# Kernel tuning notes

Hardware: AMD Instinct MI355X
Metric: run time of the kernel (lower is better)

The kernel has to match this reference:

```python
import jax, jax.numpy as jnp
import numpy as np
import math

DEPTH = 3
RATIO = 0.5
EPS = 1e-5


def _mlp_ln(h, W1, b1, W2, b2, W3, b3, g, beta):
    h = jax.nn.gelu(h @ W1 + b1, approximate=False)
    h = jax.nn.gelu(h @ W2 + b2, approximate=False)
    h = h @ W3 + b3
    mu = jnp.mean(h, axis=-1, keepdims=True)
    var = jnp.mean((h - mu) ** 2, axis=-1, keepdims=True)
    return g * (h - mu) * jax.lax.rsqrt(var + EPS) + beta


def _node_to_node(x, s, r, n, p):
    # two-way gather -> scatter_add -> MLP+LN. Row n of x_pad is a zero dummy
    # node that absorbs edges dropped by pooling (fixed-size, jit-friendly).
    x_pad = jnp.concatenate([x, jnp.zeros((1, x.shape[1]), x.dtype)], axis=0)
    msg = x_pad[jnp.concatenate([s, r])]            # [2E, C]
    recv = jnp.concatenate([r, s])                  # [2E]
    agg = jax.ops.segment_sum(msg, recv, num_segments=n + 1)[:n]
    return _mlp_ln(agg, *p)


def _forward(x, senders, receivers, pool_w, down_p, up_p):
    s, r = senders, receivers
    xs, edges, perms = [x], [(s, r)], []
    n = x.shape[0]
    for i in range(DEPTH):
        k = math.ceil(RATIO * n)  # PyG topk: ceil(ratio * N)
        w = pool_w[i]
        score = jnp.tanh(x @ w / jnp.linalg.norm(w))
        vals, perm = jax.lax.top_k(score, k)
        x = x[perm] * vals[:, None]
        # remap edges; dropped nodes (and old dummy n) map to new dummy k
        nmap = jnp.full((n + 1,), k, dtype=s.dtype).at[perm].set(
            jnp.arange(k, dtype=s.dtype))
        ns_, nr_ = nmap[s], nmap[r]
        invalid = (ns_ == k) | (nr_ == k)
        s = jnp.where(invalid, k, ns_)
        r = jnp.where(invalid, k, nr_)
        x = _node_to_node(x, s, r, k, down_p[i])
        if i < DEPTH - 1:
            xs.append(x)
            edges.append((s, r))
        perms.append(perm)
        n = k
    for i in range(DEPTH):
        j = DEPTH - 1 - i
        res = xs[j]
        s, r = edges[j]
        perm = perms[j]
        up = jnp.zeros_like(res).at[perm].set(x)
        x = jnp.concatenate([res, up], axis=-1)  # sum_res=False -> concat
        x = _node_to_node(x, s, r, res.shape[0], up_p[i])
    return x


def setup_inputs() -> dict:
    key = jax.random.key(0)
    ks = jax.random.split(key, 16)
    N, E, C, D = 50000, 600000, 128, DEPTH
    f32 = jnp.float32

    def lin(k, fi, fo):
        return (jax.random.normal(k, (D, fi, fo), f32) / np.sqrt(fi)).astype(f32)

    return {
        'x': jax.random.normal(ks[0], (N, C), f32),
        'senders': jax.random.randint(ks[1], (E,), 0, N, dtype=jnp.int32),
        'receivers': jax.random.randint(ks[2], (E,), 0, N, dtype=jnp.int32),
        'pool_w': jax.random.normal(ks[3], (D, C), f32),
        'down_W1': lin(ks[4], C, C), 'down_b1': jnp.zeros((D, C), f32),
        'down_W2': lin(ks[5], C, C), 'down_b2': jnp.zeros((D, C), f32),
        'down_W3': lin(ks[6], C, C), 'down_b3': jnp.zeros((D, C), f32),
        'down_g': jnp.ones((D, C), f32), 'down_beta': jnp.zeros((D, C), f32),
        'up_W1': lin(ks[7], 2 * C, C), 'up_b1': jnp.zeros((D, C), f32),
        'up_W2': lin(ks[8], C, C), 'up_b2': jnp.zeros((D, C), f32),
        'up_W3': lin(ks[9], C, C), 'up_b3': jnp.zeros((D, C), f32),
        'up_g': jnp.ones((D, C), f32), 'up_beta': jnp.zeros((D, C), f32),
    }


def reference(x, senders, receivers, pool_w,
              down_W1, down_b1, down_W2, down_b2, down_W3, down_b3,
              down_g, down_beta,
              up_W1, up_b1, up_W2, up_b2, up_W3, up_b3, up_g, up_beta):
    down_p = [(down_W1[i], down_b1[i], down_W2[i], down_b2[i],
               down_W3[i], down_b3[i], down_g[i], down_beta[i])
              for i in range(DEPTH)]
    up_p = [(up_W1[i], up_b1[i], up_W2[i], up_b2[i],
             up_W3[i], up_b3[i], up_g[i], up_beta[i])
            for i in range(DEPTH)]
    return _forward(x, senders, receivers, pool_w, down_p, up_p)
```

## Files before the change

kernel.cpp:

```cpp
#include <hip/hip_runtime.h>
#include <math.h>


typedef unsigned short u16;
typedef short bf16x8 __attribute__((ext_vector_type(8)));
typedef float f32x4 __attribute__((ext_vector_type(4)));

#define HIST_STRIDE (2 * 65536 + 512)
#define NB 128
#define NB_LOG 7
#define SUBR 5000

__device__ __forceinline__ unsigned int fkey(float f) {
  unsigned int b = __float_as_uint(f);
  return (b & 0x80000000u) ? ~b : (b | 0x80000000u);
}

__device__ __forceinline__ float gelu_f(float v) {
  return 0.5f * v * (1.0f + erff(v * 0.70710678118654752f));
}

__device__ __forceinline__ u16 f2bf(float f) {
  unsigned u = __float_as_uint(f);
  u = (u + 0x7FFFu + ((u >> 16) & 1u)) >> 16;
// ... 190 lines not shown
                                  int* __restrict__ nmap, int n, int k) {
  __shared__ int red[256];
  __shared__ int woff[4];
  int t = threadIdx.x;
  red[t] = (t < (int)blockIdx.x) ? tcnt[t] : 0;
  __syncthreads();
  for (int s = 128; s; s >>= 1) {
    if (t < s) red[t] += red[t + s];
    __syncthreads();
  }
  int blockbase = red[0];
  unsigned uT = (unsigned)meta[3];
  int tsel = meta[4];
  int i = blockIdx.x * 256 + t;
  unsigned u = (i < n) ? fkey(key[i]) : 0u;
  bool tie = (i < n) && (u == uT);
  unsigned long long m = __ballot(tie);
  int lane = t & 63, w = t >> 6;
  if (lane == 0) woff[w] = __popcll(m);
  __syncthreads();
  if (t == 0) {
    int c = 0;
    for (int q = 0; q < 4; ++q) { int v = woff[q]; woff[q] = c; c += v; }
  }
  __syncthreads();
  if (i > n) return;
  if (i == n) { nmap[n] = k; return; }
  bool sel;
  if (tie) {
    int pre = __popcll(m & ((1ull << lane) - 1ull));
    int rank = blockbase + woff[w] + pre;
    sel = (rank < tsel);
  } else {
    sel = (u > uT);
  }
  if (sel) {
    int slot = atomicAdd(&meta[5], 1);
    perm[slot] = i; vals[slot] = valt[i]; nmap[i] = slot;
  } else {
    nmap[i] = k;
  }
}

__global__ void pool_kernel(const float* __restrict__ x, const int* __restrict__ perm,
                            const float* __restrict__ vals, float* __restrict__ xp, int k) {
  int gid = blockIdx.x * 256 + threadIdx.x;
  int t = gid >> 5;
  if (t >= k) return;
  int c = (gid & 31) << 2;
  float v = vals[t];
  float4 a = *(const float4*)&x[(size_t)perm[t] * 128 + c];
  a.x *= v; a.y *= v; a.z *= v; a.w *= v;
  *(float4*)&xp[(size_t)t * 128 + c] = a;
}

__global__ void csr_count_kernel(const int* __restrict__ s, const int* __restrict__ r,
                                 int* __restrict__ H, int N, int E, int CH) {
  __shared__ int cnt[SUBR];
  int b = blockIdx.x & (NB - 1);
  int sub = blockIdx.x >> NB_LOG;
  int base = sub * SUBR;
  int top = base + SUBR; if (top > N) top = N;
  int span = top - base;
  for (int t = threadIdx.x; t < span; t += 256) cnt[t] = 0;
  __syncthreads();
  int lo = b * CH, hi = lo + CH; if (hi > E) hi = E;
  for (int e = lo + threadIdx.x; e < hi; e += 256) {
    int sv = s[e], rv = r[e];
    if ((unsigned)(rv - base) < (unsigned)span) atomicAdd(&cnt[rv - base], 1);
    if ((unsigned)(sv - base) < (unsigned)span) atomicAdd(&cnt[sv - base], 1);
  }
  __syncthreads();
  int* Hb = H + (size_t)b * N + base;
  for (int t = threadIdx.x; t < span; t += 256) Hb[t] = cnt[t];
}

__global__ void colsum_part_kernel(const int* __restrict__ H, int* __restrict__ deg,
                                   int* __restrict__ bsum, int n) {
  __shared__ int l[256];
  int i = blockIdx.x * 256 + threadIdx.x;
  int v = 0;
  if (i < n) {
#pragma unroll 4
    for (int b = 0; b < NB; ++b) v += H[(size_t)b * n + i];
    deg[i] = v;
  }
  l[threadIdx.x] = (i < n) ? v : 0;
  __syncthreads();
  for (int s = 128; s; s >>= 1) {
    if (threadIdx.x < s) l[threadIdx.x] += l[threadIdx.x + s];
    __syncthreads();
  }
  if (threadIdx.x == 0) bsum[blockIdx.x] = l[0];
}

__global__ void scanfix_kernel(const int* __restrict__ deg, const int* __restrict__ bsum,
                               int* __restrict__ off, int* __restrict__ H, int n) {
  __shared__ int red[256];
  __shared__ int l[256];
  int i = blockIdx.x * 256 + threadIdx.x;
  int t = threadIdx.x;
  red[t] = (t < (int)blockIdx.x) ? bsum[t] : 0;
  __syncthreads();
  for (int s = 128; s; s >>= 1) {
    if (t < s) red[t] += red[t + s];
    __syncthreads();
  }
  int base = red[0];
  int v = (i < n) ? deg[i] : 0;
  l[t] = v;
  __syncthreads();
#pragma unroll
  for (int s = 1; s < 256; s <<= 1) {
    int add = (t >= s) ? l[t - s] : 0;
    __syncthreads();
    l[t] += add;
    __syncthreads();
  }
  int incl = l[t];
  if (i < n) {
    int e = base + incl - v;
    off[i] = e;
    if (i == n - 1) off[n] = base + incl;
    int run = e;
#pragma unroll 4
    for (int b = 0; b < NB; ++b) {
      size_t id = (size_t)b * n + i;
      int tv = H[id];
      H[id] = run;
      run += tv;
    }
  }
}

__global__ void csr_scatter_lds_kernel(const int* __restrict__ s, const int* __restrict__ r,
                                       const int* __restrict__ H, int* __restrict__ idx,
                                       int N, int E, int CH) {
  __shared__ int cnt[SUBR];
  int b = blockIdx.x & (NB - 1);
  int sub = blockIdx.x >> NB_LOG;
  int base = sub * SUBR;
  int top = base + SUBR; if (top > N) top = N;
  int span = top - base;
  for (int t = threadIdx.x; t < span; t += 256) cnt[t] = 0;
  __syncthreads();
  int lo = b * CH, hi = lo + CH; if (hi > E) hi = E;
  const int* Hb = H + (size_t)b * N;
  for (int e = lo + threadIdx.x; e < hi; e += 256) {
    int sv = s[e], rv = r[e];
    if ((unsigned)(rv - base) < (unsigned)span) {
      int loc = atomicAdd(&cnt[rv - base], 1);
      idx[Hb[rv] + loc] = sv;
    }
    if ((unsigned)(sv - base) < (unsigned)span) {
      int loc = atomicAdd(&cnt[sv - base], 1);
      idx[Hb[sv] + loc] = rv;
    }
  }
}

__global__ void derive_deg_kernel(const int* __restrict__ permL, const int* __restrict__ nm,
                                  const int* __restrict__ offP, const int* __restrict__ idxP,
                                  int* __restrict__ deg, int k) {
  int wave = threadIdx.x >> 6, lane = threadIdx.x & 63;
  int v = blockIdx.x * 4 + wave;
  if (v >= k) return;
  int p = permL[v];
  int lo = __builtin_amdgcn_readfirstlane(offP[p]);
  int hi = __builtin_amdgcn_readfirstlane(offP[p + 1]);
  int cnt = 0;
  for (int j0 = lo; j0 < hi; j0 += 64) {
    int j = j0 + lane;
    bool ok = (j < hi) && (nm[idxP[j]] < k);
    unsigned long long msk = __ballot(ok);
    cnt += __popcll(msk);
  }
  if (lane == 0) deg[v] = cnt;
}

__global__ void derive_fill_kernel(const int* __restrict__ permL, const int* __restrict__ nm,
                                   const int* __restrict__ offP, const int* __restrict__ idxP,
                                   const int* __restrict__ offL, int* __restrict__ idxL,
                                   int k) {
  int wave = threadIdx.x >> 6, lane = threadIdx.x & 63;
  int v = blockIdx.x * 4 + wave;
  if (v >= k) return;
  int p = permL[v];
  int lo = __builtin_amdgcn_readfirstlane(offP[p]);
  int hi = __builtin_amdgcn_readfirstlane(offP[p + 1]);
  int base = __builtin_amdgcn_readfirstlane(offL[v]);
  for (int j0 = lo; j0 < hi; j0 += 64) {
    int j = j0 + lane;
    int m = k;
    if (j < hi) m = nm[idxP[j]];
    bool ok = m < k;
    unsigned long long msk = __ballot(ok);
    int rank = __popcll(msk & ((1ull << lane) - 1ull));
    if (ok) idxL[base + rank] = m;
    base += __popcll(msk);
  }
}

__global__ void scan_part_kernel(const int* __restrict__ deg, int* __restrict__ bsum, int n) {
  __shared__ int l[256];
  int i = blockIdx.x * 256 + threadIdx.x;
  l[threadIdx.x] = (i < n) ? deg[i] : 0;
  __syncthreads();
  for (int s = 128; s; s >>= 1) {
    if (threadIdx.x < s) l[threadIdx.x] += l[threadIdx.x + s];
    __syncthreads();
  }
  if (threadIdx.x == 0) bsum[blockIdx.x] = l[0];
}

__global__ void scan_final_kernel(const int* __restrict__ deg, const int* __restrict__ bsum,
                                  int* __restrict__ off, int n) {
  __shared__ int red[256];
  __shared__ int l[256];
  int i = blockIdx.x * 256 + threadIdx.x;
  int t = threadIdx.x;
  red[t] = (t < (int)blockIdx.x) ? bsum[t] : 0;
  __syncthreads();
  for (int s = 128; s; s >>= 1) {
    if (t < s) red[t] += red[t + s];
    __syncthreads();
  }
  int base = red[0];
  int v = (i < n) ? deg[i] : 0;
  l[t] = v;
  __syncthreads();
#pragma unroll
  for (int s = 1; s < 256; s <<= 1) {
    int add = (t >= s) ? l[t - s] : 0;
    __syncthreads();
    l[t] += add;
    __syncthreads();
  }
  int incl = l[t];
  if (i < n) {
    int e = base + incl - v;
    off[i] = e;
    if (i == n - 1) off[n] = base + incl;
  }
}

__global__ void idxup3_kernel(const int* __restrict__ idxA, const int* __restrict__ nmA,
                              const int* __restrict__ lenA, int* __restrict__ outA,
                              const int* __restrict__ idxB, const int* __restrict__ nmB,
                              const int* __restrict__ lenB, int* __restrict__ outB,
                              const int* __restrict__ idxC, const int* __restrict__ nmC,
                              const int* __restrict__ lenC, int* __restrict__ outC,
                              int nbSeg, int maxlen) {
  int seg = blockIdx.x / nbSeg;
  int j = (blockIdx.x - seg * nbSeg) * 256 + threadIdx.x;
  if (j >= maxlen) return;
  const int* idx; const int* nm; const int* len; int* out;
  if (seg == 0)      { idx = idxA; nm = nmA; len = lenA; out = outA; }
  else if (seg == 1) { idx = idxB; nm = nmB; len = lenB; out = outB; }
  else               { idx = idxC; nm = nmC; len = lenC; out = outC; }
  if (j >= len[0]) return;
  out[j] = nm[idx[j]];
}

__global__ void agg_kernel(const float* __restrict__ x, const int* __restrict__ off,
                           const int* __restrict__ idx, float* __restrict__ agg, int n) {
  int wave = threadIdx.x >> 6, lane = threadIdx.x & 63;
  int v = blockIdx.x * 4 + wave;
  if (v >= n) return;
  int lo = __builtin_amdgcn_readfirstlane(off[v]);
  int hi = __builtin_amdgcn_readfirstlane(off[v + 1]);
  int g = lane >> 5, sl = lane & 31;
  const float* bp = x + sl * 4;
  float4 acc = {0.f, 0.f, 0.f, 0.f};
#define ACC_F(EE)                                        \
  do {                                                   \
    float4 w_ = *(const float4*)(bp + (size_t)(EE) * 128);\
    acc.x += w_.x; acc.y += w_.y; acc.z += w_.z; acc.w += w_.w; \
  } while (0)
  int j = lo;
  for (; j + 8 <= hi; j += 8) {
    int q0 = idx[j],     q1 = idx[j + 1], q2 = idx[j + 2], q3 = idx[j + 3];
    int q4 = idx[j + 4], q5 = idx[j + 5], q6 = idx[j + 6], q7 = idx[j + 7];
    ACC_F(g ? q1 : q0);
    ACC_F(g ? q3 : q2);
    ACC_F(g ? q5 : q4);
    ACC_F(g ? q7 : q6);
  }
  for (; j + 2 <= hi; j += 2) {
    int q0 = idx[j], q1 = idx[j + 1];
    ACC_F(g ? q1 : q0);
  }
  if (j < hi) {
    int q0 = idx[j];
    if (!g) ACC_F(q0);
  }
#undef ACC_F
  acc.x += __shfl_xor(acc.x, 32, 64);
  acc.y += __shfl_xor(acc.y, 32, 64);
  acc.z += __shfl_xor(acc.z, 32, 64);
  acc.w += __shfl_xor(acc.w, 32, 64);
  if (!g) *(float4*)&agg[(size_t)v * 128 + sl * 4] = acc;
}

template <int OFS>
__global__ void agg_gather_kernel(const u16* __restrict__ tab, const int* __restrict__ idx,
                                  const int* __restrict__ off, u16* __restrict__ agg, int n) {
  int wave = threadIdx.x >> 6, lane = threadIdx.x & 63;
  int v = blockIdx.x * 4 + wave;
  if (v >= n) return;
  int lo = __builtin_amdgcn_readfirstlane(off[v]);
  int hi = __builtin_amdgcn_readfirstlane(off[v + 1]);
  int g = lane >> 4, sl = lane & 15;
  const u16* bp = tab + sl * 8;
  float4 a0 = {0.f, 0.f, 0.f, 0.f}, a1 = {0.f, 0.f, 0.f, 0.f};

#define ACC_ROW(EE)                                     \
  do {                                                  \
    uint4 wq = *(const uint4*)(bp + (size_t)(EE) * 128);\
    a0.x += __uint_as_float(wq.x << 16);                \
    a0.y += __uint_as_float(wq.x & 0xffff0000u);        \
    a0.z += __uint_as_float(wq.y << 16);                \
    a0.w += __uint_as_float(wq.y & 0xffff0000u);        \
    a1.x += __uint_as_float(wq.z << 16);                \
    a1.y += __uint_as_float(wq.z & 0xffff0000u);        \
    a1.z += __uint_as_float(wq.w << 16);                \
    a1.w += __uint_as_float(wq.w & 0xffff0000u);        \
  } while (0)

  int j = lo;
  for (; j + 16 <= hi; j += 16) {
    int e0 = idx[j + g];
    int e1 = idx[j + g + 4];
    int e2 = idx[j + g + 8];
    int e3 = idx[j + g + 12];
    ACC_ROW(e0); ACC_ROW(e1); ACC_ROW(e2); ACC_ROW(e3);
  }
  for (; j + 4 <= hi; j += 4) {
    int e0 = idx[j + g];
    ACC_ROW(e0);
  }
  int rmn = hi - j;
  if (g < rmn) {
    int e = idx[j + g];
    ACC_ROW(e);
  }
#undef ACC_ROW

  a0.x += __shfl_xor(a0.x, 16, 64);
  a0.y += __shfl_xor(a0.y, 16, 64);
  a0.z += __shfl_xor(a0.z, 16, 64);
  a0.w += __shfl_xor(a0.w, 16, 64);
  a1.x += __shfl_xor(a1.x, 16, 64);
  a1.y += __shfl_xor(a1.y, 16, 64);
  a1.z += __shfl_xor(a1.z, 16, 64);
  a1.w += __shfl_xor(a1.w, 16, 64);
  a0.x += __shfl_xor(a0.x, 32, 64);
  a0.y += __shfl_xor(a0.y, 32, 64);
  a0.z += __shfl_xor(a0.z, 32, 64);
  a0.w += __shfl_xor(a0.w, 32, 64);
  a1.x += __shfl_xor(a1.x, 32, 64);
  a1.y += __shfl_xor(a1.y, 32, 64);
  a1.z += __shfl_xor(a1.z, 32, 64);
  a1.w += __shfl_xor(a1.w, 32, 64);

  if (lane < 16) {
    bf16x8 ov;
    ov[0] = (short)f2bf(a0.x); ov[1] = (short)f2bf(a0.y);
    ov[2] = (short)f2bf(a0.z); ov[3] = (short)f2bf(a0.w);
    ov[4] = (short)f2bf(a1.x); ov[5] = (short)f2bf(a1.y);
    ov[6] = (short)f2bf(a1.z); ov[7] = (short)f2bf(a1.w);
    *(bf16x8*)&agg[(size_t)v * 256 + OFS + sl * 8] = ov;
  }
}

template <bool GELU>
__global__ __launch_bounds__(256) void gemm_kernel(const float* __restrict__ A,
                                                   const float* __restrict__ W,
                                                   const float* __restrict__ bias,
                                                   float* __restrict__ out, int n) {
  __shared__ float As[32 * 32];
  __shared__ float Ws[32 * 128];
  int t = threadIdx.x;
  int row0 = blockIdx.x * 32;
  int colg = (t & 31) << 2;
  int rowg = (t >> 5) << 2;
  float acc[4][4];
#pragma unroll
  for (int i = 0; i < 4; ++i)
#pragma unroll
    for (int j = 0; j < 4; ++j) acc[i][j] = 0.f;

  for (int k0 = 0; k0 < 128; k0 += 32) {
    __syncthreads();
    {
      int ar = t >> 3, ac = (t & 7) << 2;
      float4 av = make_float4(0.f, 0.f, 0.f, 0.f);
      if (row0 + ar < n) av = *(const float4*)&A[(size_t)(row0 + ar) * 128 + k0 + ac];
      *(float4*)&As[ar * 32 + ac] = av;
    }
#pragma unroll
    for (int l = 0; l < 4; ++l) {
      int id = t + l * 256;
      int kk = id >> 5, wc = (id & 31) << 2;
      *(float4*)&Ws[kk * 128 + wc] = *(const float4*)&W[(size_t)(k0 + kk) * 128 + wc];
    }
    __syncthreads();
#pragma unroll
    for (int kk = 0; kk < 32; kk += 4) {
      float4 wv[4];
#pragma unroll
      for (int j = 0; j < 4; ++j) wv[j] = *(const float4*)&Ws[(kk + j) * 128 + colg];
#pragma unroll
      for (int i = 0; i < 4; ++i) {
        float4 av = *(const float4*)&As[(rowg + i) * 32 + kk];
        acc[i][0] += av.x * wv[0].x + av.y * wv[1].x + av.z * wv[2].x + av.w * wv[3].x;
        acc[i][1] += av.x * wv[0].y + av.y * wv[1].y + av.z * wv[2].y + av.w * wv[3].y;
        acc[i][2] += av.x * wv[0].z + av.y * wv[1].z + av.z * wv[2].z + av.w * wv[3].z;
        acc[i][3] += av.x * wv[0].w + av.y * wv[1].w + av.z * wv[2].w + av.w * wv[3].w;
      }
    }
  }
  float4 bv = *(const float4*)&bias[colg];
#pragma unroll
  for (int i = 0; i < 4; ++i) {
    int rr = row0 + rowg + i;
    if (rr < n) {
      float4 o = make_float4(acc[i][0] + bv.x, acc[i][1] + bv.y, acc[i][2] + bv.z, acc[i][3] + bv.w);
      if (GELU) { o.x = gelu_f(o.x); o.y = gelu_f(o.y); o.z = gelu_f(o.z); o.w = gelu_f(o.w); }
      *(float4*)&out[(size_t)rr * 128 + colg] = o;
    }
  }
}

template <int K>
__global__ __launch_bounds__(256) void gemm_mfma_kernel(const u16* __restrict__ A,
                                                        const u16* __restrict__ WT,
                                                        const float* __restrict__ bias,
                                                        u16* __restrict__ out, int n) {
  __shared__ u16 As[64 * 72];
  __shared__ u16 Ws[128 * 72];
  int t = threadIdx.x;
  int lane = t & 63, wave = t >> 6;
  int row0 = blockIdx.x * 64;
  f32x4 acc[8];
#pragma unroll
  for (int i = 0; i < 8; ++i) acc[i] = (f32x4){0.f, 0.f, 0.f, 0.f};

  for (int k0 = 0; k0 < K; k0 += 64) {
    __syncthreads();
#pragma unroll
    for (int i = 0; i < 2; ++i) {
      int c = t + i * 256;
      int r = c >> 3, seg = c & 7;
      bf16x8 v = {0, 0, 0, 0, 0, 0, 0, 0};
      if (row0 + r < n) v = *(const bf16x8*)&A[(size_t)(row0 + r) * K + k0 + seg * 8];
      *(bf16x8*)&As[r * 72 + seg * 8] = v;
    }
#pragma unroll
    for (int i = 0; i < 4; ++i) {
      int c = t + i * 256;
      int r = c >> 3, seg = c & 7;
      *(bf16x8*)&Ws[r * 72 + seg * 8] = *(const bf16x8*)&WT[(size_t)r * K + k0 + seg * 8];
    }
    __syncthreads();
#pragma unroll
    for (int kk = 0; kk < 64; kk += 32) {
      bf16x8 a = *(const bf16x8*)&As[(wave * 16 + (lane & 15)) * 72 + kk + (lane >> 4) * 8];
#pragma unroll
      for (int ct = 0; ct < 8; ++ct) {
        bf16x8 b = *(const bf16x8*)&Ws[(ct * 16 + (lane & 15)) * 72 + kk + (lane >> 4) * 8];
        acc[ct] = __builtin_amdgcn_mfma_f32_16x16x32_bf16(a, b, acc[ct], 0, 0, 0);
      }
    }
  }
  int colb = lane & 15, rquad = lane >> 4;
#pragma unroll
  for (int ct = 0; ct < 8; ++ct) {
#pragma unroll
    for (int r = 0; r < 4; ++r) {
      int row = row0 + wave * 16 + rquad * 4 + r;
      if (row < n) {
        int col = ct * 16 + colb;
        out[(size_t)row * 128 + col] = f2bf(gelu_f(acc[ct][r] + bias[col]));
      }
    }
  }
}

template <bool WF32, bool WBF>
__global__ __launch_bounds__(256) void gemm_mfma_ln_kernel(
    const u16* __restrict__ A, const u16* __restrict__ WT, const float* __restrict__ bias,
    const float* __restrict__ g, const float* __restrict__ beta,
    float* __restrict__ out, u16* __restrict__ outbf, int n) {
  __shared__ u16 As[64 * 72];
  __shared__ u16 Ws[128 * 72];
  int t = threadIdx.x;
  int lane = t & 63, wave = t >> 6;
  int row0 = blockIdx.x * 64;
  f32x4 acc[8];
#pragma unroll
  for (int i = 0; i < 8; ++i) acc[i] = (f32x4){0.f, 0.f, 0.f, 0.f};

  for (int k0 = 0; k0 < 128; k0 += 64) {
    __syncthreads();
#pragma unroll
    for (int i = 0; i < 2; ++i) {
      int c = t + i * 256;
      int r = c >> 3, seg = c & 7;
      bf16x8 v = {0, 0, 0, 0, 0, 0, 0, 0};
      if (row0 + r < n) v = *(const bf16x8*)&A[(size_t)(row0 + r) * 128 + k0 + seg * 8];
      *(bf16x8*)&As[r * 72 + seg * 8] = v;
    }
#pragma unroll
    for (int i = 0; i < 4; ++i) {
      int c = t + i * 256;
      int r = c >> 3, seg = c & 7;
      *(bf16x8*)&Ws[r * 72 + seg * 8] = *(const bf16x8*)&WT[(size_t)r * 128 + k0 + seg * 8];
    }
    __syncthreads();
#pragma unroll
    for (int kk = 0; kk < 64; kk += 32) {
      bf16x8 a = *(const bf16x8*)&As[(wave * 16 + (lane & 15)) * 72 + kk + (lane >> 4) * 8];
#pragma unroll
      for (int ct = 0; ct < 8; ++ct) {
        bf16x8 b = *(const bf16x8*)&Ws[(ct * 16 + (lane & 15)) * 72 + kk + (lane >> 4) * 8];
        acc[ct] = __builtin_amdgcn_mfma_f32_16x16x32_bf16(a, b, acc[ct], 0, 0, 0);
      }
    }
  }
  int colb = lane & 15, rquad = lane >> 4;
  float bv[8], gv[8], bev[8];
#pragma unroll
  for (int ct = 0; ct < 8; ++ct) {
    int col = ct * 16 + colb;
    bv[ct] = bias[col]; gv[ct] = g[col]; bev[ct] = beta[col];
  }
#pragma unroll
  for (int r = 0; r < 4; ++r) {
    float s1 = 0.f;
#pragma unroll
    for (int ct = 0; ct < 8; ++ct) s1 += acc[ct][r] + bv[ct];
#pragma unroll
    for (int o = 1; o <= 8; o <<= 1) s1 += __shfl_xor(s1, o, 64);
    float mu = s1 * (1.0f / 128.0f);
    float s2 = 0.f;
#pragma unroll
    for (int ct = 0; ct < 8; ++ct) { float d = acc[ct][r] + bv[ct] - mu; s2 += d * d; }
#pragma unroll
    for (int o = 1; o <= 8; o <<= 1) s2 += __shfl_xor(s2, o, 64);
    float rs = rsqrtf(s2 * (1.0f / 128.0f) + 1e-5f);
    int row = row0 + wave * 16 + rquad * 4 + r;
    if (row < n) {
#pragma unroll
      for (int ct = 0; ct < 8; ++ct) {
        int col = ct * 16 + colb;
        float o = gv[ct] * (acc[ct][r] + bv[ct] - mu) * rs + bev[ct];
        if (WF32) out[(size_t)row * 128 + col] = o;
        if (WBF)  outbf[(size_t)row * 128 + col] = f2bf(o);
      }
    }
  }
}

template <bool SCORE, bool WBF>
__global__ void ln_kernel(const float* __restrict__ h, const float* __restrict__ g,
                          const float* __restrict__ beta, float* __restrict__ out,
                          u16* __restrict__ outbf, const float* __restrict__ wnext,
                          const double* __restrict__ sqn, float* __restrict__ key,
                          float* __restrict__ valt, int n) {
  int wave = threadIdx.x >> 6, lane = threadIdx.x & 63;
  int i = blockIdx.x * 4 + wave;
  if (i >= n) return;
  float2 hv = *(const float2*)&h[(size_t)i * 128 + lane * 2];
  float s = hv.x + hv.y;
  for (int o = 32; o; o >>= 1) s += __shfl_down(s, o, 64);
  float mu = __shfl(s, 0, 64) * (1.0f / 128.0f);
  float dx = hv.x - mu, dy = hv.y - mu;
  float q = dx * dx + dy * dy;
  for (int o = 32; o; o >>= 1) q += __shfl_down(q, o, 64);
  float var = __shfl(q, 0, 64) * (1.0f / 128.0f);
  float rs = rsqrtf(var + 1e-5f);
  float2 gv = *(const float2*)&g[lane * 2];
  float2 bv = *(const float2*)&beta[lane * 2];
  float2 o2; o2.x = gv.x * dx * rs + bv.x; o2.y = gv.y * dy * rs + bv.y;
  *(float2*)&out[(size_t)i * 128 + lane * 2] = o2;
  if (WBF)
    *(ushort2*)&outbf[(size_t)i * 128 + lane * 2] = make_ushort2(f2bf(o2.x), f2bf(o2.y));
  if (SCORE) {
    float2 wv = *(const float2*)&wnext[lane * 2];
    double d = (double)o2.x * wv.x + (double)o2.y * wv.y;
    for (int o = 32; o; o >>= 1) d += __shfl_down(d, o, 64);
    if (lane == 0) {
      key[i]  = (float)d;
      valt[i] = (float)tanh(d / sqn[0]);
    }
  }
}


static inline int cdiv(int a, int b) { return (a + b - 1) / b; }

extern "C" void kernel_launch(void* const* d_in, const int* in_sizes, int n_in,
                              void* d_out, int out_size, void* d_ws, size_t ws_size,
                              hipStream_t stream) {
  const float* x0   = (const float*)d_in[0];
  const int*   snd  = (const int*)d_in[1];
  const int*   rcv  = (const int*)d_in[2];
  const float* poolw = (const float*)d_in[3];
  const float* dW1 = (const float*)d_in[4];
  const float* db1 = (const float*)d_in[5];
  const float* dW2 = (const float*)d_in[6];
  const float* db2 = (const float*)d_in[7];
  const float* dW3 = (const float*)d_in[8];
  const float* db3 = (const float*)d_in[9];
  const float* dg  = (const float*)d_in[10];
  const float* dbe = (const float*)d_in[11];
  const float* uW1 = (const float*)d_in[12];
  const float* ub1 = (const float*)d_in[13];
  const float* uW2 = (const float*)d_in[14];
  const float* ub2 = (const float*)d_in[15];
  const float* uW3 = (const float*)d_in[16];
  const float* ub3 = (const float*)d_in[17];
  const float* ug  = (const float*)d_in[18];
  const float* ube = (const float*)d_in[19];

  const int N0 = in_sizes[0] / 128;
  const int E  = in_sizes[1];
  const int N1 = (N0 + 1) / 2, N2 = (N1 + 1) / 2, N3 = (N2 + 1) / 2;

  char* p = (char*)d_ws;
  auto alloc = [&](size_t bytes) -> void* {
    void* r = (void*)p;
    p += (bytes + 255) & ~(size_t)255;
    return r;
  };
  float* key  = (float*)alloc((size_t)N0 * 4);
  float* valt = (float*)alloc((size_t)N0 * 4);
  int*   histAll = (int*)alloc((size_t)3 * HIST_STRIDE * 4);
  int*   meta = (int*)alloc(64 * 4);
  int*   tcnt = (int*)alloc(512 * 4);
  int*   bsum = (int*)alloc(256 * 4);
  int*   nm1 = (int*)alloc((size_t)(N0 + 1) * 4);
  int*   nm2 = (int*)alloc((size_t)(N1 + 1) * 4);
  int*   nm3 = (int*)alloc((size_t)(N2 + 1) * 4);
  int*   perm0 = (int*)alloc((size_t)N1 * 4);
  int*   perm1 = (int*)alloc((size_t)N2 * 4);
  int*   perm2 = (int*)alloc((size_t)N3 * 4);
  float* vals  = (float*)alloc((size_t)N1 * 4);
  double* sqn  = (double*)alloc(8 * 8);
  float* x1 = (float*)alloc((size_t)N1 * 128 * 4);
  float* x2 = (float*)alloc((size_t)N2 * 128 * 4);
  float* x3 = (float*)alloc((size_t)N3 * 128 * 4);
  float* xp = (float*)alloc((size_t)N1 * 128 * 4);
  float* aggf = (float*)alloc((size_t)N1 * 128 * 4);
  float* h1f  = (float*)alloc((size_t)N1 * 128 * 4);
  float* h2f  = (float*)alloc((size_t)N1 * 128 * 4);
  u16* agg_bf = (u16*)alloc((size_t)N0 * 256 * 2);
  u16* res0_bf = (u16*)alloc((size_t)N0 * 128 * 2);
  u16* res1_bf = (u16*)alloc((size_t)N1 * 128 * 2);
  u16* res2_bf = (u16*)alloc((size_t)N2 * 128 * 2);
  u16* x3_bf   = (u16*)alloc((size_t)(N3 + 1) * 128 * 2);
  u16* xu2_bf  = (u16*)alloc((size_t)(N2 + 1) * 128 * 2);
  u16* xu1_bf  = (u16*)alloc((size_t)(N1 + 1) * 128 * 2);
  u16* wt1 = (u16*)alloc((size_t)3 * 128 * 256 * 2);
  u16* wt2 = (u16*)alloc((size_t)3 * 128 * 128 * 2);
  u16* wt3 = (u16*)alloc((size_t)3 * 128 * 128 * 2);
  int* degAll = (int*)alloc((size_t)(N0 + N1 + N2 + N3) * 4);
  int* deg0 = degAll;
  int* deg1 = degAll + N0;
  int* deg2 = deg1 + N1;
  int* deg3 = deg2 + N2;
  int* off0 = (int*)alloc((size_t)(N0 + 1) * 4);
  int* idx0 = (int*)alloc((size_t)2 * E * 4);
  int* off1 = (int*)alloc((size_t)(N1 + 1) * 4);
  int* idx1 = (int*)alloc((size_t)2 * E * 4);
  int* off2 = (int*)alloc((size_t)(N2 + 1) * 4);
  int* idx2 = (int*)alloc((size_t)2 * E * 4);
  int* off3 = (int*)alloc((size_t)(N3 + 1) * 4);
  int* idx3 = (int*)alloc((size_t)2 * E * 4);
  int* idxu0 = (int*)alloc((size_t)2 * E * 4);
  int* idxu1 = (int*)alloc((size_t)2 * E * 4);
  int* idxu2 = (int*)alloc((size_t)2 * E * 4);
  int* H = (int*)alloc((size_t)NB * N0 * 4);
  u16* h1b = (u16*)xp;
  u16* h2b = (u16*)alloc((size_t)N0 * 128 * 2);

  auto run_scan = [&](int* degB, int* offB, int n) {
    int nb = cdiv(n, 256);
    scan_part_kernel<<<nb, 256, 0, stream>>>(degB, bsum, n);
    scan_final_kernel<<<nb, 256, 0, stream>>>(degB, bsum, offB, n);
  };

  {
    int nbX = cdiv(N0 * 32, 256);
    int nHist = 3 * HIST_STRIDE;
    int nbHZ = cdiv(nHist, 256);
    preamble_kernel<<<nbX + 768 + 1 + 1 + nbHZ, 256, 0, stream>>>(
        x0, res0_bf, N0, uW1, uW2, uW3, wt1, wt2, wt3, poolw, sqn,
        x3_bf + (size_t)N3 * 128, xu2_bf + (size_t)N2 * 128,
        xu1_bf + (size_t)N1 * 128, histAll, nbX, nbHZ, nHist);
  }

  {
    int nSub = cdiv(N0, SUBR);
    int CH = cdiv(E, NB);
    int nbN = cdiv(N0, 256);
    csr_count_kernel<<<NB * nSub, 256, 0, stream>>>(snd, rcv, H, N0, E, CH);
    colsum_part_kernel<<<nbN, 256, 0, stream>>>(H, deg0, bsum, N0);
    scanfix_kernel<<<nbN, 256, 0, stream>>>(deg0, bsum, off0, H, N0);
    csr_scatter_lds_kernel<<<NB * nSub, 256, 0, stream>>>(snd, rcv, H, idx0, N0, E, CH);
  }

  auto down_step = [&](int n, int k, const float* xcur, int* permL, int* nmL,
                       float* xnext, u16* xnext_bf, int lvl,
                       const int* offP, const int* idxP,
                       int* offL, int* degL, int* idxL) {
    int nb = cdiv(n, 256);
    int* histL = histAll + (size_t)lvl * HIST_STRIDE;
    int* csum_hi = histL + 2 * 65536;
    int* csum_lo = csum_hi + 256;
    hist_hi_kernel<<<nb, 256, 0, stream>>>(key, histL, csum_hi, n);
    find_hi2_kernel<<<1, 256, 0, stream>>>(histL, csum_hi, meta, k);
    hist_lo_kernel<<<nb, 256, 0, stream>>>(key, meta, histL + 65536, csum_lo, n);
    find_lo2_kernel<<<1, 256, 0, stream>>>(histL + 65536, csum_lo, meta);
    tie_count_kernel<<<nb, 256, 0, stream>>>(key, meta, tcnt, n);
    tie_select_kernel<<<cdiv(n + 1, 256), 256, 0, stream>>>(
        key, valt, tcnt, meta, permL, vals, nmL, n, k);
    pool_kernel<<<cdiv(k * 32, 256), 256, 0, stream>>>(xcur, permL, vals, xp, k);
    derive_deg_kernel<<<cdiv(k, 4), 256, 0, stream>>>(permL, nmL, offP, idxP, degL, k);
    run_scan(degL, offL, k);
    derive_fill_kernel<<<cdiv(k, 4), 256, 0, stream>>>(permL, nmL, offP, idxP, offL, idxL, k);
    agg_kernel<<<cdiv(k, 4), 256, 0, stream>>>(xp, offL, idxL, aggf, k);
    gemm_kernel<true><<<cdiv(k, 32), 256, 0, stream>>>(
        aggf, dW1 + (size_t)lvl * 128 * 128, db1 + (size_t)lvl * 128, h1f, k);
    gemm_kernel<true><<<cdiv(k, 32), 256, 0, stream>>>(
        h1f, dW2 + (size_t)lvl * 128 * 128, db2 + (size_t)lvl * 128, h2f, k);
    gemm_kernel<false><<<cdiv(k, 32), 256, 0, stream>>>(
        h2f, dW3 + (size_t)lvl * 128 * 128, db3 + (size_t)lvl * 128, h1f, k);
    if (lvl < 2)
      ln_kernel<true, true><<<cdiv(k, 4), 256, 0, stream>>>(
          h1f, dg + (size_t)lvl * 128, dbe + (size_t)lvl * 128, xnext, xnext_bf,
          poolw + (size_t)(lvl + 1) * 128, sqn + (lvl + 1), key, valt, k);
    else
      ln_kernel<false, true><<<cdiv(k, 4), 256, 0, stream>>>(
          h1f, dg + (size_t)lvl * 128, dbe + (size_t)lvl * 128, xnext, xnext_bf,
          nullptr, nullptr, nullptr, nullptr, k);
  };

  score_kernel<<<cdiv(N0, 4), 256, 0, stream>>>(x0, poolw, key, valt, N0);
  down_step(N0, N1, x0, perm0, nm1, x1, res1_bf, 0, off0, idx0, off1, deg1, idx1);
  down_step(N1, N2, x1, perm1, nm2, x2, res2_bf, 1, off1, idx1, off2, deg2, idx2);
  down_step(N2, N3, x2, perm2, nm3, x3, x3_bf,   2, off2, idx2, off3, deg3, idx3);

  {
    int nbSeg = cdiv(2 * E, 256);
    idxup3_kernel<<<3 * nbSeg, 256, 0, stream>>>(
        idx2, nm3, off2 + N2, idxu2,
        idx1, nm2, off1 + N1, idxu1,
        idx0, nm1, off0 + N0, idxu0, nbSeg, 2 * E);
  }

  auto up_step = [&](int n, const u16* resb, const u16* xdb, int lvl,
                     const int* offL, const int* idxL, const int* idxUL,
                     bool wantF32, float* outF32, u16* outBF) {
    agg_gather_kernel<0><<<cdiv(n, 4), 256, 0, stream>>>(resb, idxL, offL, agg_bf, n);
    agg_gather_kernel<128><<<cdiv(n, 4), 256, 0, stream>>>(xdb, idxUL, offL, agg_bf, n);
    gemm_mfma_kernel<256><<<cdiv(n, 64), 256, 0, stream>>>(
        agg_bf, wt1 + (size_t)lvl * 128 * 256, ub1 + (size_t)lvl * 128, h1b, n);
    gemm_mfma_kernel<128><<<cdiv(n, 64), 256, 0, stream>>>(
        h1b, wt2 + (size_t)lvl * 128 * 128, ub2 + (size_t)lvl * 128, h2b, n);
    if (wantF32)
      gemm_mfma_ln_kernel<true, false><<<cdiv(n, 64), 256, 0, stream>>>(
          h2b, wt3 + (size_t)lvl * 128 * 128, ub3 + (size_t)lvl * 128,
          ug + (size_t)lvl * 128, ube + (size_t)lvl * 128, outF32, nullptr, n);
    else
      gemm_mfma_ln_kernel<false, true><<<cdiv(n, 64), 256, 0, stream>>>(
          h2b, wt3 + (size_t)lvl * 128 * 128, ub3 + (size_t)lvl * 128,
          ug + (size_t)lvl * 128, ube + (size_t)lvl * 128, nullptr, outBF, n);
  };

  up_step(N2, res2_bf, x3_bf,  0, off2, idx2, idxu2, false, nullptr, xu2_bf);
  up_step(N1, res1_bf, xu2_bf, 1, off1, idx1, idxu1, false, nullptr, xu1_bf);
  up_step(N0, res0_bf, xu1_bf, 2, off0, idx0, idxu0, true, (float*)d_out, nullptr);

  (void)n_in; (void)out_size; (void)ws_size;
}
```

Measured before the change: 831.2 us.

## Fuse three-layer MLP and LayerNorm into single kernels for down and up paths

The down path now runs one kernel that chains all three fp32 GEMMs, GELU, LayerNorm and the next-level score computation, keeping intermediates in shared memory. The up path does the same with bf16 MFMA, holding hidden activations in LDS instead of round-tripping through global buffers. The two gather launches per up level are also merged into one grid. This removes several launches and global reads and writes of intermediates. In exchange it uses more LDS per block, which may lower occupancy, and reduces the LayerNorm across 32 lanes with shuffles.

```diff
diff --git a/kernel.cpp b/kernel.cpp
--- a/kernel.cpp
+++ b/kernel.cpp
@@ -516,11 +516,17 @@
   if (!g) *(float4*)&agg[(size_t)v * 128 + sl * 4] = acc;
 }
 
-template <int OFS>
-__global__ void agg_gather_kernel(const u16* __restrict__ tab, const int* __restrict__ idx,
-                                  const int* __restrict__ off, u16* __restrict__ agg, int n) {
+__global__ void agg_gather2_kernel(const u16* __restrict__ tabR, const int* __restrict__ idxR,
+                                   const u16* __restrict__ tabU, const int* __restrict__ idxU,
+                                   const int* __restrict__ off, u16* __restrict__ agg,
+                                   int n, int nbHalf) {
+  bool upH = (int)blockIdx.x >= nbHalf;
+  int blk = upH ? (int)blockIdx.x - nbHalf : (int)blockIdx.x;
+  const u16* tab = upH ? tabU : tabR;
+  const int* idx = upH ? idxU : idxR;
+  int OFS = upH ? 128 : 0;
   int wave = threadIdx.x >> 6, lane = threadIdx.x & 63;
-  int v = blockIdx.x * 4 + wave;
+  int v = blk * 4 + wave;
   if (v >= n) return;
   int lo = __builtin_amdgcn_readfirstlane(off[v]);
   int hi = __builtin_amdgcn_readfirstlane(off[v + 1]);
@@ -587,11 +593,17 @@
   }
 }
 
-template <bool GELU>
-__global__ __launch_bounds__(256) void gemm_kernel(const float* __restrict__ A,
-                                                   const float* __restrict__ W,
-                                                   const float* __restrict__ bias,
-                                                   float* __restrict__ out, int n) {
+template <bool SCORE>
+__global__ __launch_bounds__(256) void mlp_down_kernel(
+    const float* __restrict__ A,
+    const float* __restrict__ W1, const float* __restrict__ b1,
+    const float* __restrict__ W2, const float* __restrict__ b2,
+    const float* __restrict__ W3, const float* __restrict__ b3,
+    const float* __restrict__ g, const float* __restrict__ beta,
+    float* __restrict__ out, u16* __restrict__ outbf,
+    const float* __restrict__ wnext, const double* __restrict__ sqn,
+    float* __restrict__ key, float* __restrict__ valt, int n) {
+  __shared__ float cur[32 * 128];
   __shared__ float As[32 * 32];
   __shared__ float Ws[32 * 128];
   int t = threadIdx.x;
@@ -599,82 +611,138 @@
   int colg = (t & 31) << 2;
   int rowg = (t >> 5) << 2;
   float acc[4][4];
-#pragma unroll
-  for (int i = 0; i < 4; ++i)
-#pragma unroll
-    for (int j = 0; j < 4; ++j) acc[i][j] = 0.f;
-
-  for (int k0 = 0; k0 < 128; k0 += 32) {
-    __syncthreads();
-    {
-      int ar = t >> 3, ac = (t & 7) << 2;
-      float4 av = make_float4(0.f, 0.f, 0.f, 0.f);
-      if (row0 + ar < n) av = *(const float4*)&A[(size_t)(row0 + ar) * 128 + k0 + ac];
-      *(float4*)&As[ar * 32 + ac] = av;
-    }
-#pragma unroll
-    for (int l = 0; l < 4; ++l) {
-      int id = t + l * 256;
-      int kk = id >> 5, wc = (id & 31) << 2;
-      *(float4*)&Ws[kk * 128 + wc] = *(const float4*)&W[(size_t)(k0 + kk) * 128 + wc];
-    }
-    __syncthreads();
-#pragma unroll
-    for (int kk = 0; kk < 32; kk += 4) {
-      float4 wv[4];
-#pragma unroll
-      for (int j = 0; j < 4; ++j) wv[j] = *(const float4*)&Ws[(kk + j) * 128 + colg];
+  const float* Wl[3] = {W1, W2, W3};
+  const float* bl[3] = {b1, b2, b3};
+#pragma unroll
+  for (int l = 0; l < 3; ++l) {
+    const float* W = Wl[l];
+#pragma unroll
+    for (int i = 0; i < 4; ++i)
+#pragma unroll
+      for (int j = 0; j < 4; ++j) acc[i][j] = 0.f;
+    for (int k0 = 0; k0 < 128; k0 += 32) {
+      __syncthreads();
+      {
+        int ar = t >> 3, ac = (t & 7) << 2;
+        float4 av;
+        if (l == 0) {
+          av = make_float4(0.f, 0.f, 0.f, 0.f);
+          if (row0 + ar < n) av = *(const float4*)&A[(size_t)(row0 + ar) * 128 + k0 + ac];
+        } else {
+          av = *(const float4*)&cur[ar * 128 + k0 + ac];
+        }
+        *(float4*)&As[ar * 32 + ac] = av;
+      }
+#pragma unroll
+      for (int ll = 0; ll < 4; ++ll) {
+        int id = t + ll * 256;
+        int kk = id >> 5, wc = (id & 31) << 2;
+        *(float4*)&Ws[kk * 128 + wc] = *(const float4*)&W[(size_t)(k0 + kk) * 128 + wc];
+      }
+      __syncthreads();
+#pragma unroll
+      for (int kk = 0; kk < 32; kk += 4) {
+        float4 wv[4];
+#pragma unroll
+        for (int j = 0; j < 4; ++j) wv[j] = *(const float4*)&Ws[(kk + j) * 128 + colg];
+#pragma unroll
+        for (int i = 0; i < 4; ++i) {
+          float4 av = *(const float4*)&As[(rowg + i) * 32 + kk];
+          acc[i][0] += av.x * wv[0].x + av.y * wv[1].x + av.z * wv[2].x + av.w * wv[3].x;
+          acc[i][1] += av.x * wv[0].y + av.y * wv[1].y + av.z * wv[2].y + av.w * wv[3].y;
+          acc[i][2] += av.x * wv[0].z + av.y * wv[1].z + av.z * wv[2].z + av.w * wv[3].z;
+          acc[i][3] += av.x * wv[0].w + av.y * wv[1].w + av.z * wv[2].w + av.w * wv[3].w;
+        }
+      }
+    }
+    float4 bv = *(const float4*)&bl[l][colg];
+    if (l < 2) {
+      __syncthreads();
 #pragma unroll
       for (int i = 0; i < 4; ++i) {
-        float4 av = *(const float4*)&As[(rowg + i) * 32 + kk];
-        acc[i][0] += av.x * wv[0].x + av.y * wv[1].x + av.z * wv[2].x + av.w * wv[3].x;
-        acc[i][1] += av.x * wv[0].y + av.y * wv[1].y + av.z * wv[2].y + av.w * wv[3].y;
-        acc[i][2] += av.x * wv[0].z + av.y * wv[1].z + av.z * wv[2].z + av.w * wv[3].z;
-        acc[i][3] += av.x * wv[0].w + av.y * wv[1].w + av.z * wv[2].w + av.w * wv[3].w;
+        float4 o = make_float4(gelu_f(acc[i][0] + bv.x), gelu_f(acc[i][1] + bv.y),
+                               gelu_f(acc[i][2] + bv.z), gelu_f(acc[i][3] + bv.w));
+        *(float4*)&cur[(rowg + i) * 128 + colg] = o;
       }
-    }
-  }
-  float4 bv = *(const float4*)&bias[colg];
+    } else {
+#pragma unroll
+      for (int i = 0; i < 4; ++i) {
+        acc[i][0] += bv.x; acc[i][1] += bv.y; acc[i][2] += bv.z; acc[i][3] += bv.w;
+      }
+    }
+  }
+  float4 gvv = *(const float4*)&g[colg];
+  float4 bev = *(const float4*)&beta[colg];
+  float4 wv4 = make_float4(0.f, 0.f, 0.f, 0.f);
+  if (SCORE) wv4 = *(const float4*)&wnext[colg];
 #pragma unroll
   for (int i = 0; i < 4; ++i) {
+    float s1 = acc[i][0] + acc[i][1] + acc[i][2] + acc[i][3];
+#pragma unroll
+    for (int o = 1; o <= 16; o <<= 1) s1 += __shfl_xor(s1, o, 64);
+    float mu = s1 * (1.0f / 128.0f);
+    float d0 = acc[i][0] - mu, d1 = acc[i][1] - mu, d2 = acc[i][2] - mu, d3 = acc[i][3] - mu;
+    float s2 = d0 * d0 + d1 * d1 + d2 * d2 + d3 * d3;
+#pragma unroll
+    for (int o = 1; o <= 16; o <<= 1) s2 += __shfl_xor(s2, o, 64);
+    float rs = rsqrtf(s2 * (1.0f / 128.0f) + 1e-5f);
     int rr = row0 + rowg + i;
+    float o0 = gvv.x * d0 * rs + bev.x;
+    float o1 = gvv.y * d1 * rs + bev.y;
+    float o2 = gvv.z * d2 * rs + bev.z;
+    float o3 = gvv.w * d3 * rs + bev.w;
     if (rr < n) {
-      float4 o = make_float4(acc[i][0] + bv.x, acc[i][1] + bv.y, acc[i][2] + bv.z, acc[i][3] + bv.w);
-      if (GELU) { o.x = gelu_f(o.x); o.y = gelu_f(o.y); o.z = gelu_f(o.z); o.w = gelu_f(o.w); }
-      *(float4*)&out[(size_t)rr * 128 + colg] = o;
-    }
-  }
-}
-
-template <int K>
-__global__ __launch_bounds__(256) void gemm_mfma_kernel(const u16* __restrict__ A,
-                                                        const u16* __restrict__ WT,
-                                                        const float* __restrict__ bias,
-                                                        u16* __restrict__ out, int n) {
+      *(float4*)&out[(size_t)rr * 128 + colg] = make_float4(o0, o1, o2, o3);
+      *(ushort4*)&outbf[(size_t)rr * 128 + colg] =
+          make_ushort4(f2bf(o0), f2bf(o1), f2bf(o2), f2bf(o3));
+    }
+    if (SCORE) {
+      double d = (double)o0 * wv4.x + (double)o1 * wv4.y +
+                 (double)o2 * wv4.z + (double)o3 * wv4.w;
+#pragma unroll
+      for (int o = 1; o <= 16; o <<= 1) d += __shfl_xor(d, o, 64);
+      if ((t & 31) == 0 && rr < n) {
+        key[rr]  = (float)d;
+        valt[rr] = (float)tanh(d / sqn[0]);
+      }
+    }
+  }
+}
+
+template <bool WF32, bool WBF>
+__global__ __launch_bounds__(256) void mlp_up_kernel(
+    const u16* __restrict__ A,
+    const u16* __restrict__ WT1, const float* __restrict__ b1,
+    const u16* __restrict__ WT2, const float* __restrict__ b2,
+    const u16* __restrict__ WT3, const float* __restrict__ b3,
+    const float* __restrict__ g, const float* __restrict__ beta,
+    float* __restrict__ out, u16* __restrict__ outbf, int n) {
   __shared__ u16 As[64 * 72];
   __shared__ u16 Ws[128 * 72];
+  __shared__ u16 cur[64 * 136];
   int t = threadIdx.x;
   int lane = t & 63, wave = t >> 6;
   int row0 = blockIdx.x * 64;
+  int colb = lane & 15, rquad = lane >> 4;
   f32x4 acc[8];
+
 #pragma unroll
   for (int i = 0; i < 8; ++i) acc[i] = (f32x4){0.f, 0.f, 0.f, 0.f};
-
-  for (int k0 = 0; k0 < K; k0 += 64) {
+  for (int k0 = 0; k0 < 256; k0 += 64) {
     __syncthreads();
 #pragma unroll
     for (int i = 0; i < 2; ++i) {
       int c = t + i * 256;
       int r = c >> 3, seg = c & 7;
       bf16x8 v = {0, 0, 0, 0, 0, 0, 0, 0};
-      if (row0 + r < n) v = *(const bf16x8*)&A[(size_t)(row0 + r) * K + k0 + seg * 8];
+      if (row0 + r < n) v = *(const bf16x8*)&A[(size_t)(row0 + r) * 256 + k0 + seg * 8];
       *(bf16x8*)&As[r * 72 + seg * 8] = v;
     }
 #pragma unroll
     for (int i = 0; i < 4; ++i) {
       int c = t + i * 256;
       int r = c >> 3, seg = c & 7;
-      *(bf16x8*)&Ws[r * 72 + seg * 8] = *(const bf16x8*)&WT[(size_t)r * K + k0 + seg * 8];
+      *(bf16x8*)&Ws[r * 72 + seg * 8] = *(const bf16x8*)&WT1[(size_t)r * 256 + k0 + seg * 8];
     }
     __syncthreads();
 #pragma unroll
@@ -687,54 +755,32 @@
       }
     }
   }
-  int colb = lane & 15, rquad = lane >> 4;
+  __syncthreads();
 #pragma unroll
   for (int ct = 0; ct < 8; ++ct) {
+    int col = ct * 16 + colb;
+    float bb = b1[col];
 #pragma unroll
     for (int r = 0; r < 4; ++r) {
-      int row = row0 + wave * 16 + rquad * 4 + r;
-      if (row < n) {
-        int col = ct * 16 + colb;
-        out[(size_t)row * 128 + col] = f2bf(gelu_f(acc[ct][r] + bias[col]));
-      }
-    }
-  }
-}
-
-template <bool WF32, bool WBF>
-__global__ __launch_bounds__(256) void gemm_mfma_ln_kernel(
-    const u16* __restrict__ A, const u16* __restrict__ WT, const float* __restrict__ bias,
-    const float* __restrict__ g, const float* __restrict__ beta,
-    float* __restrict__ out, u16* __restrict__ outbf, int n) {
-  __shared__ u16 As[64 * 72];
-  __shared__ u16 Ws[128 * 72];
-  int t = threadIdx.x;
-  int lane = t & 63, wave = t >> 6;
-  int row0 = blockIdx.x * 64;
-  f32x4 acc[8];
+      int row = wave * 16 + rquad * 4 + r;
+      cur[row * 136 + col] = f2bf(gelu_f(acc[ct][r] + bb));
+    }
+  }
+
 #pragma unroll
   for (int i = 0; i < 8; ++i) acc[i] = (f32x4){0.f, 0.f, 0.f, 0.f};
-
   for (int k0 = 0; k0 < 128; k0 += 64) {
     __syncthreads();
-#pragma unroll
-    for (int i = 0; i < 2; ++i) {
-      int c = t + i * 256;
-      int r = c >> 3, seg = c & 7;
-      bf16x8 v = {0, 0, 0, 0, 0, 0, 0, 0};
-      if (row0 + r < n) v = *(const bf16x8*)&A[(size_t)(row0 + r) * 128 + k0 + seg * 8];
-      *(bf16x8*)&As[r * 72 + seg * 8] = v;
-    }
 #pragma unroll
     for (int i = 0; i < 4; ++i) {
       int c = t + i * 256;
       int r = c >> 3, seg = c & 7;
-      *(bf16x8*)&Ws[r * 72 + seg * 8] = *(const bf16x8*)&WT[(size_t)r * 128 + k0 + seg * 8];
+      *(bf16x8*)&Ws[r * 72 + seg * 8] = *(const bf16x8*)&WT2[(size_t)r * 128 + k0 + seg * 8];
     }
     __syncthreads();
 #pragma unroll
     for (int kk = 0; kk < 64; kk += 32) {
-      bf16x8 a = *(const bf16x8*)&As[(wave * 16 + (lane & 15)) * 72 + kk + (lane >> 4) * 8];
+      bf16x8 a = *(const bf16x8*)&cur[(wave * 16 + (lane & 15)) * 136 + k0 + kk + (lane >> 4) * 8];
 #pragma unroll
       for (int ct = 0; ct < 8; ++ct) {
         bf16x8 b = *(const bf16x8*)&Ws[(ct * 16 + (lane & 15)) * 72 + kk + (lane >> 4) * 8];
@@ -742,12 +788,44 @@
       }
     }
   }
-  int colb = lane & 15, rquad = lane >> 4;
-  float bv[8], gv[8], bev[8];
+  __syncthreads();
 #pragma unroll
   for (int ct = 0; ct < 8; ++ct) {
     int col = ct * 16 + colb;
-    bv[ct] = bias[col]; gv[ct] = g[col]; bev[ct] = beta[col];
+    float bb = b2[col];
+#pragma unroll
+    for (int r = 0; r < 4; ++r) {
+      int row = wave * 16 + rquad * 4 + r;
+      cur[row * 136 + col] = f2bf(gelu_f(acc[ct][r] + bb));
+    }
+  }
+
+#pragma unroll
+  for (int i = 0; i < 8; ++i) acc[i] = (f32x4){0.f, 0.f, 0.f, 0.f};
+  for (int k0 = 0; k0 < 128; k0 += 64) {
+    __syncthreads();
+#pragma unroll
+    for (int i = 0; i < 4; ++i) {
+      int c = t + i * 256;
+      int r = c >> 3, seg = c & 7;
+      *(bf16x8*)&Ws[r * 72 + seg * 8] = *(const bf16x8*)&WT3[(size_t)r * 128 + k0 + seg * 8];
+    }
+    __syncthreads();
+#pragma unroll
+    for (int kk = 0; kk < 64; kk += 32) {
+      bf16x8 a = *(const bf16x8*)&cur[(wave * 16 + (lane & 15)) * 136 + k0 + kk + (lane >> 4) * 8];
+#pragma unroll
+      for (int ct = 0; ct < 8; ++ct) {
+        bf16x8 b = *(const bf16x8*)&Ws[(ct * 16 + (lane & 15)) * 72 + kk + (lane >> 4) * 8];
+        acc[ct] = __builtin_amdgcn_mfma_f32_16x16x32_bf16(a, b, acc[ct], 0, 0, 0);
+      }
+    }
+  }
+  float bv[8], gv[8], bev[8];
+#pragma unroll
+  for (int ct = 0; ct < 8; ++ct) {
+    int col = ct * 16 + colb;
+    bv[ct] = b3[col]; gv[ct] = g[col]; bev[ct] = beta[col];
   }
 #pragma unroll
   for (int r = 0; r < 4; ++r) {
@@ -772,41 +850,6 @@
         if (WF32) out[(size_t)row * 128 + col] = o;
         if (WBF)  outbf[(size_t)row * 128 + col] = f2bf(o);
       }
-    }
-  }
-}
-
-template <bool SCORE, bool WBF>
-__global__ void ln_kernel(const float* __restrict__ h, const float* __restrict__ g,
-                          const float* __restrict__ beta, float* __restrict__ out,
-                          u16* __restrict__ outbf, const float* __restrict__ wnext,
-                          const double* __restrict__ sqn, float* __restrict__ key,
-                          float* __restrict__ valt, int n) {
-  int wave = threadIdx.x >> 6, lane = threadIdx.x & 63;
-  int i = blockIdx.x * 4 + wave;
-  if (i >= n) return;
-  float2 hv = *(const float2*)&h[(size_t)i * 128 + lane * 2];
-  float s = hv.x + hv.y;
-  for (int o = 32; o; o >>= 1) s += __shfl_down(s, o, 64);
-  float mu = __shfl(s, 0, 64) * (1.0f / 128.0f);
-  float dx = hv.x - mu, dy = hv.y - mu;
-  float q = dx * dx + dy * dy;
-  for (int o = 32; o; o >>= 1) q += __shfl_down(q, o, 64);
-  float var = __shfl(q, 0, 64) * (1.0f / 128.0f);
-  float rs = rsqrtf(var + 1e-5f);
-  float2 gv = *(const float2*)&g[lane * 2];
-  float2 bv = *(const float2*)&beta[lane * 2];
-  float2 o2; o2.x = gv.x * dx * rs + bv.x; o2.y = gv.y * dy * rs + bv.y;
-  *(float2*)&out[(size_t)i * 128 + lane * 2] = o2;
-  if (WBF)
-    *(ushort2*)&outbf[(size_t)i * 128 + lane * 2] = make_ushort2(f2bf(o2.x), f2bf(o2.y));
-  if (SCORE) {
-    float2 wv = *(const float2*)&wnext[lane * 2];
-    double d = (double)o2.x * wv.x + (double)o2.y * wv.y;
-    for (int o = 32; o; o >>= 1) d += __shfl_down(d, o, 64);
-    if (lane == 0) {
-      key[i]  = (float)d;
-      valt[i] = (float)tanh(d / sqn[0]);
     }
   }
 }
@@ -867,8 +910,6 @@
   float* x3 = (float*)alloc((size_t)N3 * 128 * 4);
   float* xp = (float*)alloc((size_t)N1 * 128 * 4);
   float* aggf = (float*)alloc((size_t)N1 * 128 * 4);
-  float* h1f  = (float*)alloc((size_t)N1 * 128 * 4);
-  float* h2f  = (float*)alloc((size_t)N1 * 128 * 4);
   u16* agg_bf = (u16*)alloc((size_t)N0 * 256 * 2);
   u16* res0_bf = (u16*)alloc((size_t)N0 * 128 * 2);
   u16* res1_bf = (u16*)alloc((size_t)N1 * 128 * 2);
@@ -896,14 +937,6 @@
   int* idxu1 = (int*)alloc((size_t)2 * E * 4);
   int* idxu2 = (int*)alloc((size_t)2 * E * 4);
   int* H = (int*)alloc((size_t)NB * N0 * 4);
-  u16* h1b = (u16*)xp;
-  u16* h2b = (u16*)alloc((size_t)N0 * 128 * 2);
-
-  auto run_scan = [&](int* degB, int* offB, int n) {
-    int nb = cdiv(n, 256);
-    scan_part_kernel<<<nb, 256, 0, stream>>>(degB, bsum, n);
-    scan_final_kernel<<<nb, 256, 0, stream>>>(degB, bsum, offB, n);
-  };
 
   {
     int nbX = cdiv(N0 * 32, 256);
@@ -924,6 +957,12 @@
     scanfix_kernel<<<nbN, 256, 0, stream>>>(deg0, bsum, off0, H, N0);
     csr_scatter_lds_kernel<<<NB * nSub, 256, 0, stream>>>(snd, rcv, H, idx0, N0, E, CH);
   }
+
+  auto run_scan = [&](int* degB, int* offB, int n) {
+    int nb = cdiv(n, 256);
+    scan_part_kernel<<<nb, 256, 0, stream>>>(degB, bsum, n);
+    scan_final_kernel<<<nb, 256, 0, stream>>>(degB, bsum, offB, n);
+  };
 
   auto down_step = [&](int n, int k, const float* xcur, int* permL, int* nmL,
                        float* xnext, u16* xnext_bf, int lvl,
@@ -945,20 +984,23 @@
     run_scan(degL, offL, k);
     derive_fill_kernel<<<cdiv(k, 4), 256, 0, stream>>>(permL, nmL, offP, idxP, offL, idxL, k);
     agg_kernel<<<cdiv(k, 4), 256, 0, stream>>>(xp, offL, idxL, aggf, k);
-    gemm_kernel<true><<<cdiv(k, 32), 256, 0, stream>>>(
-        aggf, dW1 + (size_t)lvl * 128 * 128, db1 + (size_t)lvl * 128, h1f, k);
-    gemm_kernel<true><<<cdiv(k, 32), 256, 0, stream>>>(
-        h1f, dW2 + (size_t)lvl * 128 * 128, db2 + (size_t)lvl * 128, h2f, k);
-    gemm_kernel<false><<<cdiv(k, 32), 256, 0, stream>>>(
-        h2f, dW3 + (size_t)lvl * 128 * 128, db3 + (size_t)lvl * 128, h1f, k);
     if (lvl < 2)
-      ln_kernel<true, true><<<cdiv(k, 4), 256, 0, stream>>>(
-          h1f, dg + (size_t)lvl * 128, dbe + (size_t)lvl * 128, xnext, xnext_bf,
-          poolw + (size_t)(lvl + 1) * 128, sqn + (lvl + 1), key, valt, k);
+      mlp_down_kernel<true><<<cdiv(k, 32), 256, 0, stream>>>(
+          aggf,
+          dW1 + (size_t)lvl * 128 * 128, db1 + (size_t)lvl * 128,
+          dW2 + (size_t)lvl * 128 * 128, db2 + (size_t)lvl * 128,
+          dW3 + (size_t)lvl * 128 * 128, db3 + (size_t)lvl * 128,
+          dg + (size_t)lvl * 128, dbe + (size_t)lvl * 128,
+          xnext, xnext_bf, poolw + (size_t)(lvl + 1) * 128, sqn + (lvl + 1),
+          key, valt, k);
     else
-      ln_kernel<false, true><<<cdiv(k, 4), 256, 0, stream>>>(
-          h1f, dg + (size_t)lvl * 128, dbe + (size_t)lvl * 128, xnext, xnext_bf,
-          nullptr, nullptr, nullptr, nullptr, k);
+      mlp_down_kernel<false><<<cdiv(k, 32), 256, 0, stream>>>(
+          aggf,
+          dW1 + (size_t)lvl * 128 * 128, db1 + (size_t)lvl * 128,
+          dW2 + (size_t)lvl * 128 * 128, db2 + (size_t)lvl * 128,
+          dW3 + (size_t)lvl * 128 * 128, db3 + (size_t)lvl * 128,
+          dg + (size_t)lvl * 128, dbe + (size_t)lvl * 128,
+          xnext, xnext_bf, nullptr, nullptr, nullptr, nullptr, k);
   };
 
   score_kernel<<<cdiv(N0, 4), 256, 0, stream>>>(x0, poolw, key, valt, N0);
@@ -977,20 +1019,25 @@
   auto up_step = [&](int n, const u16* resb, const u16* xdb, int lvl,
                      const int* offL, const int* idxL, const int* idxUL,
                      bool wantF32, float* outF32, u16* outBF) {
-    agg_gather_kernel<0><<<cdiv(n, 4), 256, 0, stream>>>(resb, idxL, offL, agg_bf, n);
-    agg_gather_kernel<128><<<cdiv(n, 4), 256, 0, stream>>>(xdb, idxUL, offL, agg_bf, n);
-    gemm_mfma_kernel<256><<<cdiv(n, 64), 256, 0, stream>>>(
-        agg_bf, wt1 + (size_t)lvl * 128 * 256, ub1 + (size_t)lvl * 128, h1b, n);
-    gemm_mfma_kernel<128><<<cdiv(n, 64), 256, 0, stream>>>(
-        h1b, wt2 + (size_t)lvl * 128 * 128, ub2 + (size_t)lvl * 128, h2b, n);
+    int nbh = cdiv(n, 4);
+    agg_gather2_kernel<<<2 * nbh, 256, 0, stream>>>(
+        resb, idxL, xdb, idxUL, offL, agg_bf, n, nbh);
     if (wantF32)
-      gemm_mfma_ln_kernel<true, false><<<cdiv(n, 64), 256, 0, stream>>>(
-          h2b, wt3 + (size_t)lvl * 128 * 128, ub3 + (size_t)lvl * 128,
-          ug + (size_t)lvl * 128, ube + (size_t)lvl * 128, outF32, nullptr, n);
+      mlp_up_kernel<true, false><<<cdiv(n, 64), 256, 0, stream>>>(
+          agg_bf,
+          wt1 + (size_t)lvl * 128 * 256, ub1 + (size_t)lvl * 128,
+          wt2 + (size_t)lvl * 128 * 128, ub2 + (size_t)lvl * 128,
+          wt3 + (size_t)lvl * 128 * 128, ub3 + (size_t)lvl * 128,
+          ug + (size_t)lvl * 128, ube + (size_t)lvl * 128,
+          outF32, nullptr, n);
     else
-      gemm_mfma_ln_kernel<false, true><<<cdiv(n, 64), 256, 0, stream>>>(
-          h2b, wt3 + (size_t)lvl * 128 * 128, ub3 + (size_t)lvl * 128,
-          ug + (size_t)lvl * 128, ube + (size_t)lvl * 128, nullptr, outBF, n);
+      mlp_up_kernel<false, true><<<cdiv(n, 64), 256, 0, stream>>>(
+          agg_bf,
+          wt1 + (size_t)lvl * 128 * 256, ub1 + (size_t)lvl * 128,
+          wt2 + (size_t)lvl * 128 * 128, ub2 + (size_t)lvl * 128,
+          wt3 + (size_t)lvl * 128 * 128, ub3 + (size_t)lvl * 128,
+          ug + (size_t)lvl * 128, ube + (size_t)lvl * 128,
+          nullptr, outBF, n);
   };
 
   up_step(N2, res2_bf, x3_bf,  0, off2, idx2, idxu2, false, nullptr, xu2_bf);
```

Result: no change. 821.1 us (-1.2%).
